# Kernel optimization log

Hardware: AMD Instinct MI355X
Metric: run time of the kernel (lower is better)

## Reference

```python
import jax, jax.numpy as jnp
import numpy as np

C_I, C_T, NUM_HEADS = 128, 256, 8
EPS = 1e-5

def conv3d1(x, W, b):
    # 1x1x1 conv: x (b,c,D,H,W), W (o,c), b (o,)
    return jnp.einsum('oc,bcdhw->bodhw', W, x) + b[None, :, None, None, None]

def conv1d1(x, W, b):
    # kernel_size=1 conv: x (b,c,l), W (o,c), b (o,)
    return jnp.einsum('oc,bcl->bol', W, x) + b[None, :, None]

def inorm3d(x):
    # InstanceNorm3d(affine=False): normalize over spatial dims, biased var
    m = jnp.mean(x, axis=(2, 3, 4), keepdims=True)
    v = jnp.var(x, axis=(2, 3, 4), keepdims=True)
    return (x - m) * jax.lax.rsqrt(v + EPS)

def setup_inputs() -> dict:
    key = jax.random.key(0)
    ks = jax.random.split(key, 20)
    B, D, H, W, L = 2, 48, 48, 48, 20
    s = 0.05
    inp = {
        'img_in': jax.random.normal(ks[0], (B, C_I, D, H, W), jnp.float32),
        'lang_in': jax.random.normal(ks[1], (B, C_T, L), jnp.float32),
        'Wq': jax.random.normal(ks[2], (C_I, C_I), jnp.float32) * s,
        'bq': jnp.zeros((C_I,), jnp.float32),
        'Wk': jax.random.normal(ks[3], (C_I, C_T), jnp.float32) * s,
        'bk': jnp.zeros((C_I,), jnp.float32),
        'Wv': jax.random.normal(ks[4], (C_I, C_T), jnp.float32) * s,
        'bv': jnp.zeros((C_I,), jnp.float32),
        'Wpw': jax.random.normal(ks[5], (C_I, C_I), jnp.float32) * s,
        'bpw': jnp.zeros((C_I,), jnp.float32),
        'Wpi': jax.random.normal(ks[6], (C_I, C_I), jnp.float32) * s,
        'bpi': jnp.zeros((C_I,), jnp.float32),
        'Wpo': jax.random.normal(ks[7], (C_I, C_I), jnp.float32) * s,
        'bpo': jnp.zeros((C_I,), jnp.float32),
        'Wg1': jax.random.normal(ks[8], (C_I, C_I), jnp.float32) * s,
        'bg1': jnp.zeros((C_I,), jnp.float32),
        'Wg2': jax.random.normal(ks[9], (C_I, C_I), jnp.float32) * s,
        'bg2': jnp.zeros((C_I,), jnp.float32),
    }
    return inp

def reference(img_in, lang_in, Wq, bq, Wk, bk, Wv, bv, Wpw, bpw, Wpi, bpi,
              Wpo, bpo, Wg1, bg1, Wg2, bg2):
    b = img_in.shape[0]
    d = int(np.prod(img_in.shape[-3:]))
    l = lang_in.shape[-1]
    hd = C_I // NUM_HEADS
    # lang_mask=None path -> all-ones mask (additive term is zero but kept faithful)
    mask = jnp.ones((b, 1, l), img_in.dtype)

    # query: conv3d(1x1)+InstanceNorm -> (b, heads, d, hd)
    q = inorm3d(conv3d1(img_in, Wq, bq)).reshape(b, C_I, d)
    q = q.transpose(0, 2, 1).reshape(b, d, NUM_HEADS, hd).transpose(0, 2, 1, 3)
    # key/value: conv1d(k=1) masked -> (b, heads, hd, l)
    k = (conv1d1(lang_in, Wk, bk) * mask).reshape(b, NUM_HEADS, hd, l)
    v = (conv1d1(lang_in, Wv, bv) * mask).reshape(b, NUM_HEADS, hd, l)

    scale = (C_I / NUM_HEADS) ** (-0.5)
    sim = jnp.einsum('bhdc,bhcl->bhdl', q, k) * scale
    sim = sim + (10000.0 * mask[:, :, None, :] - 10000.0)  # (b,1,1,l) broadcast
    attn = jax.nn.softmax(sim, axis=-1)
    x = jnp.einsum('bhdl,bhcl->bhdc', attn, v)              # (b,heads,d,hd)
    x = x.transpose(0, 2, 1, 3).reshape(b, d, C_I)
    # faithful to torch .permute(0,2,1).permute(0,2,1).view_as(img_in):
    # reshape (b, d, c_i) flat buffer into (b, c_i, D, H, W)
    x_img = x.reshape(img_in.shape)

    skip = inorm3d(conv3d1(img_in, Wpi, bpi))
    weight = inorm3d(conv3d1(x_img, Wpw, bpw))
    out = jax.nn.relu(conv3d1(skip * weight, Wpo, bpo))
    gate = jnp.tanh(conv3d1(jax.nn.relu(conv3d1(out, Wg1, bg1)), Wg2, bg2))
    return out * gate
```

## Files before the change

### kernel.cpp

```cpp
#include <hip/hip_runtime.h>
#include <cstdint>
#include <cstddef>

#define PSP 110592
#define NCH 128
#define NB  2
#define CPW 68
#define TPB 4
static constexpr float EPSV = 1e-5f;

typedef short bf16x8 __attribute__((ext_vector_type(8)));
typedef float f32x4  __attribute__((ext_vector_type(4)));

static __device__ __forceinline__ short f2bf(float f) {
    uint32_t u = __builtin_bit_cast(uint32_t, f);
    u += 0x7FFF + ((u >> 16) & 1);
    return (short)(u >> 16);
}
static __device__ __forceinline__ float bf2float(short s) {
    uint32_t u = ((uint32_t)(uint16_t)s) << 16;
    return __builtin_bit_cast(float, u);
}
static __device__ __forceinline__ float bfLO(uint32_t w) {
    return __builtin_bit_cast(float, w << 16);
}
static __device__ __forceinline__ float bfHI(uint32_t w) {
    return __builtin_bit_cast(float, w & 0xffff0000u);
}
static __device__ __forceinline__ uint32_t pk2f(float lo, float hi) {
    return (uint32_t)(uint16_t)f2bf(lo) | ((uint32_t)(uint16_t)f2bf(hi) << 16);
}
static __device__ __forceinline__ uint32_t pk2s(short lo, short hi) {
    return (uint32_t)(uint16_t)lo | ((uint32_t)(uint16_t)hi << 16);
}
static __device__ __forceinline__ int swzb(int p) {
    return (((p & 7) ^ ((p >> 3) & 7)) << 4);
}

__global__ __launch_bounds__(256) void kv_kernel(
    const float* __restrict__ lang,
    const float* __restrict__ Wk, const float* __restrict__ bk,
    const float* __restrict__ Wv, const float* __restrict__ bv,
    float* __restrict__ kout, float* __restrict__ vout)
{
    int gid = blockIdx.x * 256 + threadIdx.x;
    int sel = gid / 5120;
    int r   = gid % 5120;
    int b   = r / 2560;
    int o   = (r % 2560) / 20;
    int l   = r % 20;
    const float* W  = sel ? Wv : Wk;
    const float* bb = sel ? bv : bk;
    const float* lg = lang + b * 256 * 20 + l;
    float acc = bb[o];
    #pragma unroll 8
    for (int c = 0; c < 256; ++c)
        acc = fmaf(W[o * 256 + c], lg[c * 20], acc);
    (sel ? vout : kout)[b * 2560 + o * 20 + l] = acc;
}

__global__ __launch_bounds__(256) void wprep_kernel(
    const float* __restrict__ w0, const float* __restrict__ w1,
    const float* __restrict__ w2, const float* __restrict__ w3,
    const float* __restrict__ w4, const float* __restrict__ w5,
    short* __restrict__ wt)
{
    const int m = blockIdx.x >> 4, s = blockIdx.x & 15;
    const float* src = w0;
    if (m == 1) src = w1; else if (m == 2) src = w2; else if (m == 3) src = w3;
    else if (m == 4) src = w4; else if (m == 5) src = w5;
    short* dst = wt + m * NCH * NCH;
    const int i0 = s * 1024 + threadIdx.x * 4;
    f32x4 v = *(const f32x4*)(src + i0);
    *(uint2*)(dst + i0) = make_uint2(pk2f(v[0], v[1]), pk2f(v[2], v[3]));
}

__global__ __launch_bounds__(256) void knprep_kernel(
    const float* __restrict__ qs, const float* __restrict__ qs2,
    const float* __restrict__ kbuf,
    float* __restrict__ knb, float* __restrict__ cbb)
{
    __shared__ float mq[128], rqs[128], knl[2560];
    const int t = threadIdx.x, b = blockIdx.x;
    if (t < 128) {
        float m = qs[b * 128 + t] * (1.0f / PSP);
        float v = qs2[b * 128 + t] * (1.0f / PSP) - m * m;
        mq[t] = m;
        rqs[t] = rsqrtf(v + EPSV) * 0.25f;
    }
    __syncthreads();
    for (int e = t; e < 2560; e += 256) {
        int c = e / 20;
        float kv = rqs[c] * kbuf[b * 2560 + e];
        knl[e] = kv;
        knb[b * 2560 + e] = kv;
    }
    __syncthreads();
    if (t < 160) {
        int h = t / 20, l = t % 20;
        float s = 0.0f;
        #pragma unroll
        for (int i = 0; i < 16; ++i)
            s = fmaf(mq[h * 16 + i], knl[(h * 16 + i) * 20 + l], s);
        cbb[b * 160 + t] = s;
    }
}

struct PackW { uint32_t lo[8], hi[8]; };

static __device__ __forceinline__ void ldpack_f32(const float* src, PackW& w) {
    const int t = threadIdx.x;
    const float* s = src + (size_t)(4 * (t >> 3)) * PSP + (t & 7) * 8;
    f32x4 r0a = *(const f32x4*)s,             r0b = *(const f32x4*)(s + 4);
    f32x4 r1a = *(const f32x4*)(s + PSP),     r1b = *(const f32x4*)(s + PSP + 4);
    f32x4 r2a = *(const f32x4*)(s + 2 * PSP), r2b = *(const f32x4*)(s + 2 * PSP + 4);
    f32x4 r3a = *(const f32x4*)(s + 3 * PSP), r3b = *(const f32x4*)(s + 3 * PSP + 4);
    #pragma unroll
    for (int j = 0; j < 4; ++j) {
        w.lo[j]     = pk2f(r0a[j], r1a[j]);
        w.lo[4 + j] = pk2f(r0b[j], r1b[j]);
        w.hi[j]     = pk2f(r2a[j], r3a[j]);
        w.hi[4 + j] = pk2f(r2b[j], r3b[j]);
    }
}
static __device__ __forceinline__ void ldpack_b16(const short* src, PackW& w) {
    const int t = threadIdx.x;
    const short* s = src + (size_t)(4 * (t >> 3)) * PSP + (t & 7) * 8;
    bf16x8 r0 = *(const bf16x8*)s;
    bf16x8 r1 = *(const bf16x8*)(s + PSP);
    bf16x8 r2 = *(const bf16x8*)(s + 2 * PSP);
    bf16x8 r3 = *(const bf16x8*)(s + 3 * PSP);
    #pragma unroll
    for (int j = 0; j < 8; ++j) { w.lo[j] = pk2s(r0[j], r1[j]); w.hi[j] = pk2s(r2[j], r3[j]); }
}
static __device__ __forceinline__ void ldpack_g4(const short* skip, const short* wgt,
        const float nm[4][NCH], PackW& w) {
    const int t = threadIdx.x;
    const int c = 4 * (t >> 3), p0 = (t & 7) * 8;
    const short* s = skip + (size_t)c * PSP + p0;
    const short* g = wgt  + (size_t)c * PSP + p0;
    bf16x8 s0 = *(const bf16x8*)s,             s1 = *(const bf16x8*)(s + PSP);
    bf16x8 s2 = *(const bf16x8*)(s + 2 * PSP), s3 = *(const bf16x8*)(s + 3 * PSP);
    bf16x8 g0 = *(const bf16x8*)g,             g1 = *(const bf16x8*)(g + PSP);
    bf16x8 g2 = *(const bf16x8*)(g + 2 * PSP), g3 = *(const bf16x8*)(g + 3 * PSP);
    float mA[4], rA[4], mB[4], rB[4];
    #pragma unroll
    for (int r = 0; r < 4; ++r) {
        mA[r] = nm[0][c + r]; rA[r] = nm[1][c + r];
        mB[r] = nm[2][c + r]; rB[r] = nm[3][c + r];
    }
    #pragma unroll
    for (int j = 0; j < 8; ++j) {
        float v0 = ((bf2float(s0[j]) - mA[0]) * rA[0]) * ((bf2float(g0[j]) - mB[0]) * rB[0]);
        float v1 = ((bf2float(s1[j]) - mA[1]) * rA[1]) * ((bf2float(g1[j]) - mB[1]) * rB[1]);
        float v2 = ((bf2float(s2[j]) - mA[2]) * rA[2]) * ((bf2float(g2[j]) - mB[2]) * rB[2]);
        float v3 = ((bf2float(s3[j]) - mA[3]) * rA[3]) * ((bf2float(g3[j]) - mB[3]) * rB[3]);
        w.lo[j] = pk2f(v0, v1);
        w.hi[j] = pk2f(v2, v3);
    }
}
static __device__ __forceinline__ void stage(char* STGb, const PackW& w) {
    const int t = threadIdx.x;
    const int c8 = (t >> 3) * 8, p0 = (t & 7) * 8;
    #pragma unroll
    for (int j = 0; j < 8; ++j) {
        int byte = (p0 + j) * 256 + c8;
        byte ^= ((j ^ (t & 7)) << 4);
        *(uint2*)(STGb + byte) = make_uint2(w.lo[j], w.hi[j]);
    }
}

static __device__ __forceinline__ void load_afrag16(const short* __restrict__ W16,
                                                    int wid, int lane, bf16x8 af[2][4]) {
    const int orow = wid * 32 + (lane & 15);
    const int cb   = (lane >> 4) * 8;
    #pragma unroll
    for (int mt = 0; mt < 2; ++mt)
        #pragma unroll
        for (int kt = 0; kt < 4; ++kt)
            af[mt][kt] = *(const bf16x8*)(W16 + (size_t)(orow + mt * 16) * NCH + kt * 32 + cb);
}

static __device__ __forceinline__ void run_mfmaX(const char* STGb, const bf16x8 af[2][4],
                                                 f32x4 acc[2][4], int lane) {
    const int l15 = lane & 15, kh = lane >> 4;
    #pragma unroll
    for (int nt = 0; nt < 4; ++nt) {
        const int p = nt * 16 + l15;
        const int sw = swzb(p);
        bf16x8 bf[4];
        #pragma unroll
        for (int kt = 0; kt < 4; ++kt)
            bf[kt] = *(const bf16x8*)(STGb + ((p * 256 + kt * 64 + kh * 16) ^ sw));
        #pragma unroll
        for (int kt = 0; kt < 4; ++kt) {
            acc[0][nt] = __builtin_amdgcn_mfma_f32_16x16x32_bf16(af[0][kt], bf[kt], acc[0][nt], 0, 0, 0);
            acc[1][nt] = __builtin_amdgcn_mfma_f32_16x16x32_bf16(af[1][kt], bf[kt], acc[1][nt], 0, 0, 0);
        }
    }
}
static __device__ __forceinline__ void zero_acc(f32x4 acc[2][4]) {
    #pragma unroll
    for (int m = 0; m < 2; ++m)
        #pragma unroll
        for (int n = 0; n < 4; ++n) acc[m][n] = (f32x4)0.0f;
}
static __device__ __forceinline__ void write_LCp(uint32_t* LCp, const f32x4 acc[2][4],
                                                 int wid, int lane) {
    const int l15 = lane & 15, og = wid * 32 + (lane >> 4) * 4;
    #pragma unroll
    for (int mt = 0; mt < 2; ++mt)
        #pragma unroll
        for (int nt = 0; nt < 4; ++nt) {
            const int o2 = (og >> 1) + mt * 8, p = nt * 16 + l15;
            f32x4 a = acc[mt][nt];
            LCp[o2 * CPW + p]       = pk2f(a[0], a[1]);
            LCp[(o2 + 1) * CPW + p] = pk2f(a[2], a[3]);
        }
}
template<bool RELU, bool STATS>
static __device__ __forceinline__ void epi2(const uint32_t* LCp, const float* __restrict__ bias,
        short* __restrict__ dst, float sS[4], float sQ[4])
{
    const int t = threadIdx.x;
    #pragma unroll
    for (int r = 0; r < 4; ++r) {
        const int u = r * 256 + t, o = u >> 3, ch = u & 7, hi = o & 1;
        const float bia = bias[o];
        const uint32_t* src = LCp + (o >> 1) * CPW + ch * 8;
        uint4 wa = *(const uint4*)src;
        uint4 wb = *(const uint4*)(src + 4);
        uint32_t ww[8] = {wa.x, wa.y, wa.z, wa.w, wb.x, wb.y, wb.z, wb.w};
        float v[8];
        #pragma unroll
        for (int j = 0; j < 8; ++j) v[j] = (hi ? bfHI(ww[j]) : bfLO(ww[j])) + bia;
        if (RELU) {
            #pragma unroll
            for (int j = 0; j < 8; ++j) v[j] = fmaxf(v[j], 0.0f);
        }
        bf16x8 s8;
        #pragma unroll
        for (int j = 0; j < 8; ++j) s8[j] = f2bf(v[j]);
        *(bf16x8*)(dst + (size_t)o * PSP + ch * 8) = s8;
        if (STATS) {
            float s = 0.0f, q = 0.0f;
            #pragma unroll
            for (int j = 0; j < 8; ++j) { s += v[j]; q += v[j] * v[j]; }
            sS[r] += s; sQ[r] += q;
        }
    }
}
static __device__ __forceinline__ void flush_stats(const float sS[4], const float sQ[4],
        float* __restrict__ s_sum, float* __restrict__ s_sq)
{
    const int t = threadIdx.x;
    #pragma unroll
    for (int r = 0; r < 4; ++r) {
        float s = sS[r], q = sQ[r];
        s += __shfl_xor(s, 1); q += __shfl_xor(q, 1);
        s += __shfl_xor(s, 2); q += __shfl_xor(q, 2);
        s += __shfl_xor(s, 4); q += __shfl_xor(q, 4);
        if ((t & 7) == 0) {
            atomicAdd(&s_sum[r * 32 + (t >> 3)], s);
            atomicAdd(&s_sq [r * 32 + (t >> 3)], q);
        }
    }
}

__global__ __launch_bounds__(256) void g12_kernel(
    const float* __restrict__ img, const short* __restrict__ w16,
    const float* __restrict__ bq, const float* __restrict__ bpi,
    short* __restrict__ qout, short* __restrict__ sout,
    float* __restrict__ qs, float* __restrict__ qs2,
    float* __restrict__ ss, float* __restrict__ ss2)
{
    __shared__ __align__(16) char STGb[16384];
    __shared__ __align__(16) uint32_t LCp[64 * CPW];

    const int t = threadIdx.x, lane = t & 63, wid = t >> 6;
    const int b = blockIdx.y;
    const size_t bbase = (size_t)b * NCH * PSP;
    const int pbase = blockIdx.x * (64 * TPB);
    const int sb = b * NCH;

    bf16x8 afq[2][4], afp[2][4];
    load_afrag16(w16, wid, lane, afq);
    load_afrag16(w16 + NCH * NCH, wid, lane, afp);

    float qS[4] = {0, 0, 0, 0}, qQ[4] = {0, 0, 0, 0};
    float sS[4] = {0, 0, 0, 0}, sQ[4] = {0, 0, 0, 0};

    PackW w;
    ldpack_f32(img + bbase + pbase, w);

    for (int i = 0; i < TPB; ++i) {
        const int pblk = pbase + i * 64;
        stage(STGb, w);
        __syncthreads();
        if (i + 1 < TPB) ldpack_f32(img + bbase + pblk + 64, w);
        f32x4 acc[2][4];
        zero_acc(acc);
        run_mfmaX(STGb, afq, acc, lane);
        write_LCp(LCp, acc, wid, lane);
        __syncthreads();
        epi2<false, true>(LCp, bq, qout + bbase + pblk, qS, qQ);
        zero_acc(acc);
        run_mfmaX(STGb, afp, acc, lane);
        __syncthreads();
        write_LCp(LCp, acc, wid, lane);
        __syncthreads();
        epi2<false, true>(LCp, bpi, sout + bbase + pblk, sS, sQ);
    }
    flush_stats(qS, qQ, qs + sb, qs2 + sb);
    flush_stats(sS, sQ, ss + sb, ss2 + sb);
}

__global__ __launch_bounds__(256) void g3_kernel(
    const short* __restrict__ x, const short* __restrict__ w16,
    const float* __restrict__ bpw, short* __restrict__ wout,
    float* __restrict__ wsu, float* __restrict__ ws2)
{
    __shared__ __align__(16) char STGb[16384];
    __shared__ __align__(16) uint32_t LCp[64 * CPW];

    const int t = threadIdx.x, lane = t & 63, wid = t >> 6;
    const int b = blockIdx.y;
    const size_t bbase = (size_t)b * NCH * PSP;
    const int pbase = blockIdx.x * (64 * TPB);
    const int sb = b * NCH;

    bf16x8 af[2][4];
    load_afrag16(w16, wid, lane, af);
    float wS[4] = {0, 0, 0, 0}, wQ[4] = {0, 0, 0, 0};

    PackW w;
    ldpack_b16(x + bbase + pbase, w);

    for (int i = 0; i < TPB; ++i) {
        const int pblk = pbase + i * 64;
        stage(STGb, w);
        __syncthreads();
        if (i + 1 < TPB) ldpack_b16(x + bbase + pblk + 64, w);
        f32x4 acc[2][4];
        zero_acc(acc);
        run_mfmaX(STGb, af, acc, lane);
        write_LCp(LCp, acc, wid, lane);
        __syncthreads();
        epi2<false, true>(LCp, bpw, wout + bbase + pblk, wS, wQ);
    }
    flush_stats(wS, wQ, wsu + sb, ws2 + sb);
}

__global__ __launch_bounds__(256) void g4_kernel(
    const short* __restrict__ skip, const short* __restrict__ wgt,
    const float* __restrict__ sA, const float* __restrict__ sA2,
    const float* __restrict__ sB, const float* __restrict__ sB2,
    const short* __restrict__ w16, const float* __restrict__ bpo,
    short* __restrict__ outp)
{
    __shared__ __align__(16) char STGb[16384];
    __shared__ __align__(16) uint32_t LCp[64 * CPW];
    __shared__ float nm[4][NCH];

    const int t = threadIdx.x, lane = t & 63, wid = t >> 6;
    const int b = blockIdx.y;
    const size_t bbase = (size_t)b * NCH * PSP;
    const int pbase = blockIdx.x * (64 * TPB);

    if (t < NCH) {
        float m = sA[b * NCH + t] * (1.0f / PSP);
        float v = sA2[b * NCH + t] * (1.0f / PSP) - m * m;
        nm[0][t] = m; nm[1][t] = rsqrtf(v + EPSV);
    } else {
        int c = t - NCH;
        float m = sB[b * NCH + c] * (1.0f / PSP);
        float v = sB2[b * NCH + c] * (1.0f / PSP) - m * m;
        nm[2][c] = m; nm[3][c] = rsqrtf(v + EPSV);
    }
    bf16x8 af[2][4];
    load_afrag16(w16, wid, lane, af);
    __syncthreads();

    PackW w;
    ldpack_g4(skip + bbase + pbase, wgt + bbase + pbase, nm, w);
    float dS[4], dQ[4];

    for (int i = 0; i < TPB; ++i) {
        const int pblk = pbase + i * 64;
        stage(STGb, w);
        __syncthreads();
        if (i + 1 < TPB)
            ldpack_g4(skip + bbase + pblk + 64, wgt + bbase + pblk + 64, nm, w);
        f32x4 acc[2][4];
        zero_acc(acc);
        run_mfmaX(STGb, af, acc, lane);
        write_LCp(LCp, acc, wid, lane);
        __syncthreads();
        epi2<true, false>(LCp, bpo, outp + bbase + pblk, dS, dQ);
    }
}

__global__ __launch_bounds__(256) void g56_kernel(
    const short* __restrict__ outb, const short* __restrict__ w16g1,
    const float* __restrict__ bg1, const short* __restrict__ w16g2,
    const float* __restrict__ bg2, float* __restrict__ fin)
{
    __shared__ __align__(16) char STGb[16384];
    __shared__ __align__(16) char RTL[64 * CPW * 4];

    const int t = threadIdx.x, lane = t & 63, wid = t >> 6;
    const int b = blockIdx.y;
    const size_t bbase = (size_t)b * NCH * PSP;
    const int pbase = blockIdx.x * (64 * TPB);

    bf16x8 af1[2][4], af2[2][4];
    load_afrag16(w16g1, wid, lane, af1);
    load_afrag16(w16g2, wid, lane, af2);

    float bg1v[2][4];
    {
        const int og = wid * 32 + (lane >> 4) * 4;
        #pragma unroll
        for (int mt = 0; mt < 2; ++mt)
            #pragma unroll
            for (int r = 0; r < 4; ++r) bg1v[mt][r] = bg1[og + mt * 16 + r];
    }

    PackW w;
    ldpack_b16(outb + bbase + pbase, w);

    for (int i = 0; i < TPB; ++i) {
        const int pblk = pbase + i * 64;
        stage(STGb, w);
        __syncthreads();
        if (i + 1 < TPB) ldpack_b16(outb + bbase + pblk + 64, w);
        f32x4 acc[2][4];
        zero_acc(acc);
        run_mfmaX(STGb, af1, acc, lane);
        {
            const int l15 = lane & 15, og = wid * 32 + (lane >> 4) * 4;
            #pragma unroll
            for (int mt = 0; mt < 2; ++mt)
                #pragma unroll
                for (int nt = 0; nt < 4; ++nt) {
                    const int o = og + mt * 16, p = nt * 16 + l15;
                    const int sw = swzb(p);
                    f32x4 a = acc[mt][nt];
                    float z0 = fmaxf(a[0] + bg1v[mt][0], 0.0f);
                    float z1 = fmaxf(a[1] + bg1v[mt][1], 0.0f);
                    float z2 = fmaxf(a[2] + bg1v[mt][2], 0.0f);
                    float z3 = fmaxf(a[3] + bg1v[mt][3], 0.0f);
                    *(uint32_t*)(RTL + ((p * 256 + o * 2) ^ sw))     = pk2f(z0, z1);
                    *(uint32_t*)(RTL + ((p * 256 + o * 2 + 4) ^ sw)) = pk2f(z2, z3);
                }
        }
        __syncthreads();
        zero_acc(acc);
        run_mfmaX(RTL, af2, acc, lane);
        __syncthreads();
        write_LCp((uint32_t*)RTL, acc, wid, lane);
        __syncthreads();
        {
            const uint32_t* LCp = (const uint32_t*)RTL;
            float* dst = fin + bbase + pblk;
            #pragma unroll
            for (int r = 0; r < 4; ++r) {
                const int u = r * 256 + t, o2 = u >> 4, ch = u & 15;
                const float b0 = bg2[2 * o2], b1 = bg2[2 * o2 + 1];
                uint4 lc = *(const uint4*)(LCp + o2 * CPW + ch * 4);
                uint32_t lw[4] = {lc.x, lc.y, lc.z, lc.w};
                f32x4 oA, oB;
                #pragma unroll
                for (int j = 0; j < 4; ++j) {
                    const int p = ch * 4 + j;
                    uint32_t mw = *(const uint32_t*)(STGb + ((p * 256 + o2 * 4) ^ swzb(p)));
                    oA[j] = bfLO(mw) * tanhf(bfLO(lw[j]) + b0);
                    oB[j] = bfHI(mw) * tanhf(bfHI(lw[j]) + b1);
                }
                *(f32x4*)(dst + (size_t)(2 * o2) * PSP + ch * 4)     = oA;
                *(f32x4*)(dst + (size_t)(2 * o2 + 1) * PSP + ch * 4) = oB;
            }
        }
        __syncthreads();
    }
}

__global__ __launch_bounds__(256) void attn3_kernel(
    const short* __restrict__ qpre, const float* __restrict__ knb,
    const float* __restrict__ cbb, const float* __restrict__ vbuf,
    short* __restrict__ xout)
{
    __shared__ __align__(16) uint32_t QX[64 * 65];
    __shared__ float KN[2560], VV[2560], CB[160];

    const int t = threadIdx.x;
    const int b = blockIdx.y;
    const int pblk = blockIdx.x * 64;
    const size_t bbase = (size_t)b * NCH * PSP;

    {
        const float* kn = knb + b * 2560;
        const float* vv = vbuf + b * 2560;
        #pragma unroll
        for (int e = t; e < 2560; e += 256) { KN[e] = kn[e]; VV[e] = vv[e]; }
        if (t < 160) CB[t] = cbb[b * 160 + t];
    }
    {
        const int c2 = t >> 2, p0 = (t & 3) * 16;
        const short* s0 = qpre + bbase + (size_t)(2 * c2) * PSP + pblk + p0;
        bf16x8 a0 = *(const bf16x8*)s0,         a1 = *(const bf16x8*)(s0 + 8);
        bf16x8 b0 = *(const bf16x8*)(s0 + PSP), b1 = *(const bf16x8*)(s0 + PSP + 8);
        uint32_t w[16];
        #pragma unroll
        for (int k = 0; k < 8; ++k) { w[k] = pk2s(a0[k], b0[k]); w[8 + k] = pk2s(a1[k], b1[k]); }
        uint32_t* base = QX + c2 * 65 + p0;
        #pragma unroll
        for (int k = 0; k < 8; ++k) *(uint2*)(base + 2 * k) = make_uint2(w[2 * k], w[2 * k + 1]);
    }
    __syncthreads();

    const int p = t & 63, h0 = t >> 6;
    uint32_t qw[16];
    #pragma unroll
    for (int i = 0; i < 8; ++i) {
        qw[i]     = QX[(h0 * 8 + i) * 65 + p];
        qw[8 + i] = QX[((h0 + 4) * 8 + i) * 65 + p];
    }
    __syncthreads();

    #pragma unroll 1
    for (int hh = 0; hh < 2; ++hh) {
        const int h = h0 + hh * 4;
        const int c0 = h * 16;
        float sim[20];
        #pragma unroll
        for (int l = 0; l < 20; ++l) sim[l] = -CB[h * 20 + l];
        #pragma unroll
        for (int i = 0; i < 8; ++i) {
            const uint32_t w = qw[hh * 8 + i];
            const float qlo = bfLO(w), qhi = bfHI(w);
            const float* k0 = KN + (c0 + 2 * i) * 20;
            #pragma unroll
            for (int l = 0; l < 20; ++l)
                sim[l] = fmaf(qlo, k0[l], fmaf(qhi, k0[20 + l], sim[l]));
        }
        float mx = sim[0];
        #pragma unroll
        for (int l = 1; l < 20; ++l) mx = fmaxf(mx, sim[l]);
        float se = 0.0f;
        #pragma unroll
        for (int l = 0; l < 20; ++l) { float e = __expf(sim[l] - mx); sim[l] = e; se += e; }
        const float inv = 1.0f / se;
        #pragma unroll
        for (int i = 0; i < 8; ++i) {
            const float* v0 = VV + (c0 + 2 * i) * 20;
            float x0 = 0.0f, x1 = 0.0f;
            #pragma unroll
            for (int l = 0; l < 20; ++l) {
                x0 = fmaf(sim[l], v0[l], x0);
                x1 = fmaf(sim[l], v0[20 + l], x1);
            }
            QX[p * 65 + h * 8 + i] = pk2f(x0 * inv, x1 * inv);
        }
    }
    __syncthreads();

    {
        const int lane = t & 63, w = t >> 6;
        uint32_t* gdst = (uint32_t*)(xout + bbase + (size_t)pblk * NCH);
        #pragma unroll
        for (int j = 0; j < 4; ++j) {
            const int pp = w * 4 + j * 16 + (lane >> 4);
            const int cw = (lane & 15) * 4;
            const uint32_t* s = QX + pp * 65 + cw;
            *(uint4*)(gdst + pp * 64 + cw) = make_uint4(s[0], s[1], s[2], s[3]);
        }
    }
}

extern "C" void kernel_launch(void* const* d_in, const int* in_sizes, int n_in,
                              void* d_out, int out_size, void* d_ws, size_t ws_size,
                              hipStream_t stream)
{
    const float* img  = (const float*)d_in[0];
    const float* lang = (const float*)d_in[1];
    const float* Wq   = (const float*)d_in[2];
    const float* bq   = (const float*)d_in[3];
    const float* Wk   = (const float*)d_in[4];
    const float* bk   = (const float*)d_in[5];
    const float* Wv   = (const float*)d_in[6];
    const float* bv   = (const float*)d_in[7];
    const float* Wpw  = (const float*)d_in[8];
    const float* bpw  = (const float*)d_in[9];
    const float* Wpi  = (const float*)d_in[10];
    const float* bpi  = (const float*)d_in[11];
    const float* Wpo  = (const float*)d_in[12];
    const float* bpo  = (const float*)d_in[13];
    const float* Wg1  = (const float*)d_in[14];
    const float* bg1  = (const float*)d_in[15];
    const float* Wg2  = (const float*)d_in[16];
    const float* bg2  = (const float*)d_in[17];
    float* outp = (float*)d_out;

    const size_t N = (size_t)NB * NCH * PSP;
    const size_t needed = 3 * N * sizeof(short) + 6 * NCH * NCH * sizeof(short)
                        + (3 * 2 * 2560 + 2 * 160 + 6 * 256) * sizeof(float);
    if (ws_size < needed) return;

    short* bufA = (short*)d_ws;
    short* bufB = bufA + N;
    short* bufC = bufB + N;
    short* wt16 = bufC + N;
    float* kbuf = (float*)(wt16 + 6 * NCH * NCH);
    float* vbuf = kbuf + 2 * 2560;
    float* knb  = vbuf + 2 * 2560;
    float* cbb  = knb + 2 * 2560;
    float* st   = cbb + 2 * 160;
    float* qs   = st;
    float* qs2  = st + 256;
    float* ss   = st + 512;
    float* ss2  = st + 768;
    float* wsu  = st + 1024;
    float* ws2  = st + 1280;

    (void)hipMemsetAsync(st, 0, 6 * 256 * sizeof(float), stream);
    kv_kernel<<<dim3(40), dim3(256), 0, stream>>>(lang, Wk, bk, Wv, bv, kbuf, vbuf);
    wprep_kernel<<<dim3(96), dim3(256), 0, stream>>>(Wq, Wpi, Wpw, Wpo, Wg1, Wg2, wt16);

    const dim3 gg(PSP / (64 * TPB), NB), gb(256);

    g12_kernel<<<gg, gb, 0, stream>>>(img, wt16, bq, bpi, bufA, bufC, qs, qs2, ss, ss2);
    knprep_kernel<<<dim3(NB), dim3(256), 0, stream>>>(qs, qs2, kbuf, knb, cbb);
    attn3_kernel<<<dim3(PSP / 64, NB), gb, 0, stream>>>(bufA, knb, cbb, vbuf, bufB);
    g3_kernel<<<gg, gb, 0, stream>>>(bufB, wt16 + 2 * NCH * NCH, bpw, bufA, wsu, ws2);
    g4_kernel<<<gg, gb, 0, stream>>>(bufC, bufA, ss, ss2, wsu, ws2,
                                     wt16 + 3 * NCH * NCH, bpo, bufB);
    g56_kernel<<<gg, gb, 0, stream>>>(bufB, wt16 + 4 * NCH * NCH, bg1,
                                      wt16 + 5 * NCH * NCH, bg2, outp);
}
```

Measured before the change: 321.8 us.

## Store Q projection in MFMA-fragment tile layout and skip LDS epilogue

The query projection epilogue now adds bias, packs to bf16 and writes accumulators directly from registers in a per-64-pixel tiled fragment layout. It accumulates instance-norm statistics per lane with shuffle reductions and atomics, which removes the LDS round-trip and one barrier. The attention kernel then loads each Q tile with contiguous 16-byte copies and reads it through a fragment-offset index function instead of gathering two channel rows. The trade is a custom intermediate layout coupled across both kernels, and LDS reads with a new access pattern that may cause bank conflicts.

```diff
diff --git a/kernel.cpp b/kernel.cpp
--- a/kernel.cpp
+++ b/kernel.cpp
@@ -35,6 +35,14 @@
 }
 static __device__ __forceinline__ int swzb(int p) {
     return (((p & 7) ^ ((p >> 3) & 7)) << 4);
+}
+static __device__ __forceinline__ int qfrag_off(int c2, int p) {
+    const int c = c2 * 2;
+    const int widp = c >> 5, cp = c & 31;
+    const int mt = (cp >> 4) & 1, lane4 = (cp >> 2) & 3, j = (cp >> 1) & 1;
+    const int tp = widp * 64 + lane4 * 16 + (p & 15);
+    const int m  = (mt * 4 + (p >> 4)) * 2 + j;
+    return (m >> 2) * 1024 + tp * 4 + (m & 3);
 }
 
 __global__ __launch_bounds__(256) void kv_kernel(
@@ -287,8 +295,17 @@
     load_afrag16(w16, wid, lane, afq);
     load_afrag16(w16 + NCH * NCH, wid, lane, afp);
 
-    float qS[4] = {0, 0, 0, 0}, qQ[4] = {0, 0, 0, 0};
+    const int og0 = wid * 32 + (lane >> 4) * 4;
+    float bqv[2][4];
+    #pragma unroll
+    for (int mt = 0; mt < 2; ++mt)
+        #pragma unroll
+        for (int r = 0; r < 4; ++r) bqv[mt][r] = bq[og0 + mt * 16 + r];
+
+    float qS[2][4] = {{0,0,0,0},{0,0,0,0}}, qQ[2][4] = {{0,0,0,0},{0,0,0,0}};
     float sS[4] = {0, 0, 0, 0}, sQ[4] = {0, 0, 0, 0};
+
+    uint32_t* qtb = (uint32_t*)qout + (size_t)b * ((size_t)NCH * PSP / 2);
 
     PackW w;
     ldpack_f32(img + bbase + pbase, w);
@@ -301,9 +318,27 @@
         f32x4 acc[2][4];
         zero_acc(acc);
         run_mfmaX(STGb, afq, acc, lane);
-        write_LCp(LCp, acc, wid, lane);
-        __syncthreads();
-        epi2<false, true>(LCp, bq, qout + bbase + pblk, qS, qQ);
+        {
+            uint32_t q16[16];
+            #pragma unroll
+            for (int mt = 0; mt < 2; ++mt)
+                #pragma unroll
+                for (int nt = 0; nt < 4; ++nt) {
+                    f32x4 a = acc[mt][nt];
+                    float v0 = a[0] + bqv[mt][0], v1 = a[1] + bqv[mt][1];
+                    float v2 = a[2] + bqv[mt][2], v3 = a[3] + bqv[mt][3];
+                    q16[(mt * 4 + nt) * 2]     = pk2f(v0, v1);
+                    q16[(mt * 4 + nt) * 2 + 1] = pk2f(v2, v3);
+                    qS[mt][0] += v0; qS[mt][1] += v1; qS[mt][2] += v2; qS[mt][3] += v3;
+                    qQ[mt][0] += v0 * v0; qQ[mt][1] += v1 * v1;
+                    qQ[mt][2] += v2 * v2; qQ[mt][3] += v3 * v3;
+                }
+            uint32_t* qt = qtb + (size_t)(pblk >> 6) * 4096;
+            #pragma unroll
+            for (int k = 0; k < 4; ++k)
+                *(uint4*)(qt + k * 1024 + t * 4) =
+                    make_uint4(q16[4 * k], q16[4 * k + 1], q16[4 * k + 2], q16[4 * k + 3]);
+        }
         zero_acc(acc);
         run_mfmaX(STGb, afp, acc, lane);
         __syncthreads();
@@ -311,7 +346,20 @@
         __syncthreads();
         epi2<false, true>(LCp, bpi, sout + bbase + pblk, sS, sQ);
     }
-    flush_stats(qS, qQ, qs + sb, qs2 + sb);
+    #pragma unroll
+    for (int mt = 0; mt < 2; ++mt)
+        #pragma unroll
+        for (int r = 0; r < 4; ++r) {
+            float s = qS[mt][r], q = qQ[mt][r];
+            s += __shfl_xor(s, 1); q += __shfl_xor(q, 1);
+            s += __shfl_xor(s, 2); q += __shfl_xor(q, 2);
+            s += __shfl_xor(s, 4); q += __shfl_xor(q, 4);
+            s += __shfl_xor(s, 8); q += __shfl_xor(q, 8);
+            if ((lane & 15) == 0) {
+                atomicAdd(&qs [sb + og0 + mt * 16 + r], s);
+                atomicAdd(&qs2[sb + og0 + mt * 16 + r], q);
+            }
+        }
     flush_stats(sS, sQ, ss + sb, ss2 + sb);
 }
 
@@ -506,16 +554,11 @@
         if (t < 160) CB[t] = cbb[b * 160 + t];
     }
     {
-        const int c2 = t >> 2, p0 = (t & 3) * 16;
-        const short* s0 = qpre + bbase + (size_t)(2 * c2) * PSP + pblk + p0;
-        bf16x8 a0 = *(const bf16x8*)s0,         a1 = *(const bf16x8*)(s0 + 8);
-        bf16x8 b0 = *(const bf16x8*)(s0 + PSP), b1 = *(const bf16x8*)(s0 + PSP + 8);
-        uint32_t w[16];
-        #pragma unroll
-        for (int k = 0; k < 8; ++k) { w[k] = pk2s(a0[k], b0[k]); w[8 + k] = pk2s(a1[k], b1[k]); }
-        uint32_t* base = QX + c2 * 65 + p0;
-        #pragma unroll
-        for (int k = 0; k < 8; ++k) *(uint2*)(base + 2 * k) = make_uint2(w[2 * k], w[2 * k + 1]);
+        const uint32_t* qt = (const uint32_t*)qpre + (size_t)b * ((size_t)NCH * PSP / 2)
+                           + (size_t)blockIdx.x * 4096;
+        #pragma unroll
+        for (int k = 0; k < 4; ++k)
+            *(uint4*)(QX + k * 1024 + t * 4) = *(const uint4*)(qt + k * 1024 + t * 4);
     }
     __syncthreads();
 
@@ -523,8 +566,8 @@
     uint32_t qw[16];
     #pragma unroll
     for (int i = 0; i < 8; ++i) {
-        qw[i]     = QX[(h0 * 8 + i) * 65 + p];
-        qw[8 + i] = QX[((h0 + 4) * 8 + i) * 65 + p];
+        qw[i]     = QX[qfrag_off(h0 * 8 + i, p)];
+        qw[8 + i] = QX[qfrag_off((h0 + 4) * 8 + i, p)];
     }
     __syncthreads();
 
```

New measurement: 352.9 us. 1.1x slower.
